# Performance work log

Measured on AMD Instinct MI355X. Metric: run time of the kernel, lower is better.

Reference implementation:

```python
import jax, jax.numpy as jnp
import numpy as np

B, L, C = 4, 2048, 1024
H = 16
D = C // H  # head_dim = 64


def _rope(t, cos, sin):
    # t: [B, H, L, D]; cos/sin: [L, D//2] broadcast to [1, 1, L, D//2]
    te = t[..., ::2]
    to = t[..., 1::2]
    c = cos[None, None]
    s = sin[None, None]
    re = te * c - to * s
    ro = te * s + to * c
    # interleave even/odd back: [..., D//2, 2] -> [..., D]
    return jnp.stack([re, ro], axis=-1).reshape(t.shape)


def setup_inputs() -> dict:
    key = jax.random.key(0)
    ks = jax.random.split(key, 5)
    x = jax.random.normal(ks[0], (B, L, C), dtype=jnp.float32)
    # rotary phases: theta_i = 10000^(-2i/D), angles = pos * theta
    inv_freq = 1.0 / (10000.0 ** (np.arange(0, D, 2, dtype=np.float32) / D))
    ang = np.arange(L, dtype=np.float32)[:, None] * inv_freq[None, :]  # [L, D//2]
    cos = jnp.asarray(np.cos(ang))
    sin = jnp.asarray(np.sin(ang))
    w_qkv = jax.random.normal(ks[1], (3 * C, C), dtype=jnp.float32) * (C ** -0.5)
    w_proj = jax.random.normal(ks[2], (C, C), dtype=jnp.float32) * (C ** -0.5)
    b_proj = jnp.zeros((C,), dtype=jnp.float32)
    return {"x": x, "cos": cos, "sin": sin, "w_qkv": w_qkv, "w_proj": w_proj, "b_proj": b_proj}


def reference(x, cos, sin, w_qkv, w_proj, b_proj):
    Bx, Lx, Cx = x.shape
    # QKV projection (torch Linear: y = x @ W.T), then split heads
    qkv = jnp.einsum("blc,fc->blf", x, w_qkv)  # [B, L, 3C]
    qkv = qkv.reshape(Bx, Lx, 3, H, D).transpose(2, 0, 3, 1, 4)  # [3, B, H, L, D]
    q, k, v = qkv[0], qkv[1], qkv[2]
    q = _rope(q, cos, sin)
    k = _rope(k, cos, sin)
    # scaled dot-product attention, non-causal
    scale = D ** -0.5
    scores = jnp.einsum("bhqd,bhkd->bhqk", q, k) * scale
    attn = jax.nn.softmax(scores, axis=-1)
    o = jnp.einsum("bhqk,bhkd->bhqd", attn, v)  # [B, H, L, D]
    o = o.transpose(0, 2, 1, 3).reshape(Bx, Lx, Cx)
    return jnp.einsum("blc,fc->blf", o, w_proj) + b_proj
```

## Files before the change

### kernel.cpp

```cpp
#include <hip/hip_runtime.h>
#include <hip/hip_bf16.h>
#include <cstdint>


typedef unsigned short u16;
typedef __attribute__((ext_vector_type(8))) short bf16x8;
typedef __attribute__((ext_vector_type(4))) float f32x4;
typedef __attribute__((ext_vector_type(2))) unsigned int u32x2;

#define GLD16(g, l)                                                            \
  __builtin_amdgcn_global_load_lds(                                            \
      (const __attribute__((address_space(1))) void*)(g),                      \
      (__attribute__((address_space(3))) void*)(l), 16, 0, 0)

static __device__ __forceinline__ u16 f32_bf16(float f) {
  union { float f; unsigned u; } v; v.f = f;
  unsigned r = v.u + 0x7FFFu + ((v.u >> 16) & 1u);
  return (u16)(r >> 16);
}
static __device__ __forceinline__ float bf16_f32(u16 h) {
  union { unsigned u; float f; } v; v.u = ((unsigned)h) << 16;
  return v.f;
}
static __device__ __forceinline__ unsigned pack_rne(float a, float b) {
  union { float f; unsigned u; } x, y; x.f = a; y.f = b;
  unsigned ua = x.u + 0x7FFFu + ((x.u >> 16) & 1u);
  unsigned ub = y.u + 0x7FFFu + ((y.u >> 16) & 1u);
  return (ua >> 16) | (ub & 0xFFFF0000u);
}
static __device__ __forceinline__ unsigned pack_bf16_hw(float a, float b) {
  float2 t; t.x = a; t.y = b;
  __hip_bfloat162 h = __float22bfloat162_rn(t);
  union { __hip_bfloat162 h; unsigned u; } c; c.h = h;
  return c.u;
}

__global__ __launch_bounds__(256) void convert_all(
    const void* __restrict__ x, const void* __restrict__ wq,
    const void* __restrict__ wp, const void* __restrict__ cs,
    const void* __restrict__ sn, const void* __restrict__ bs,
    u16* __restrict__ xb, u16* __restrict__ wqb, u16* __restrict__ wpb,
    u16* __restrict__ cb, u16* __restrict__ sb, u16* __restrict__ bb) {
  const unsigned f32mode = (((const unsigned*)cs)[0] == 0x3F800000u);
  int blk = blockIdx.x;
  if (blk >= 12288 && blk < 12416) {
    const void* src = (blk < 12352) ? cs : sn;
    u16* dst = (blk < 12352) ? cb : sb;
    int i = (blk - ((blk < 12352) ? 12288 : 12352)) * 256 + threadIdx.x;
    u16 e[4];
    if (f32mode) {
      float4 v = ((const float4*)src)[i];
      const float* vf = (const float*)&v;
#pragma unroll
      for (int c = 0; c < 4; c++) e[c] = f32_bf16(vf[c]);
    } else {
      uint2 v = ((const uint2*)src)[i];
      e[0] = (u16)(v.x & 0xFFFFu); e[1] = (u16)(v.x >> 16);
      e[2] = (u16)(v.y & 0xFFFFu); e[3] = (u16)(v.y >> 16);
    }
#pragma unroll
    for (int c = 0; c < 4; c++) {
      int E = i * 4 + c;
      dst[(E & 31) * 2048 + (E >> 5)] = e[c];
    }
    return;
  }
  const void* src; u16* dst; int i0, n4;
  bool is_wq = false;
  if (blk < 8192)       { src = x;  dst = xb;  i0 = blk;         n4 = 2097152; }
  else if (blk < 11264) { src = wq; dst = wqb; i0 = blk - 8192;  n4 = 786432; is_wq = true; }
  else if (blk < 12288) { src = wp; dst = wpb; i0 = blk - 11264; n4 = 262144; }
  else                  { src = bs; dst = bb;  i0 = blk - 12416; n4 = 256; }
  int i = i0 * 256 + threadIdx.x;
  if (i >= n4) return;
  int si = i;
  if (is_wq) {
    int f = i >> 8, c4 = i & 255;
    if (f < 2048) {
      int loc = f & 63;
      int srcf = (f & ~63) | ((loc < 32) ? (2 * loc) : (2 * (loc - 32) + 1));
      si = srcf * 256 + c4;
    }
  }
  if (f32mode) {
    float4 v = ((const float4*)src)[si];
    uint2 o;
    o.x = pack_rne(v.x, v.y);
    o.y = pack_rne(v.z, v.w);
    ((uint2*)dst)[i] = o;
  } else {
    ((uint2*)dst)[i] = ((const uint2*)src)[si];
  }
}

static __device__ __forceinline__ void gemm_mainloop(
    const u16* __restrict__ A, const u16* __restrict__ Bm, int K,
    int m0, int n0, u16* As, u16* Bs, f32x4 acc[4][4]) {
  const int tid  = threadIdx.x;
  const int lane = tid & 63;
  const int wave = tid >> 6;
  const int n16  = lane & 15;
  const int quad = lane >> 4;
  const int wm = (wave >> 1) * 64;
  const int wn = (wave & 1) * 64;
  const u16* ag = A  + (size_t)(m0 + wave * 16 + (lane >> 2)) * K + (lane & 3) * 8;
  const u16* bg = Bm + (size_t)(n0 + wave * 16 + (lane >> 2)) * K + (lane & 3) * 8;
  u16* al = As + wave * (16 * 32);
  u16* bl = Bs + wave * (16 * 32);
  GLD16(ag, al);
  GLD16(ag + (size_t)64 * K, al + 64 * 32);
  GLD16(bg, bl);
  GLD16(bg + (size_t)64 * K, bl + 64 * 32);
  for (int kt = 0; kt < K; kt += 32) {
    const int buf = (kt >> 5) & 1;
    __syncthreads();
    if (kt + 32 < K) {
      const int nb = buf ^ 1;
      GLD16(ag + kt + 32, al + nb * 4096);
      GLD16(ag + (size_t)64 * K + kt + 32, al + nb * 4096 + 64 * 32);
      GLD16(bg + kt + 32, bl + nb * 4096);
      GLD16(bg + (size_t)64 * K + kt + 32, bl + nb * 4096 + 64 * 32);
    }
    const u16* as = As + buf * 4096;
    const u16* bs = Bs + buf * 4096;
    bf16x8 af[4], bf[4];
#pragma unroll
    for (int i = 0; i < 4; i++)
      af[i] = *(const bf16x8*)(as + (wm + i * 16 + n16) * 32 + quad * 8);
#pragma unroll
    for (int j = 0; j < 4; j++)
      bf[j] = *(const bf16x8*)(bs + (wn + j * 16 + n16) * 32 + quad * 8);
#pragma unroll
    for (int i = 0; i < 4; i++)
#pragma unroll
      for (int j = 0; j < 4; j++)
        acc[i][j] = __builtin_amdgcn_mfma_f32_16x16x32_bf16(af[i], bf[j], acc[i][j], 0, 0, 0);
  }
}

__global__ __launch_bounds__(256) void gemm_qkv(
    const u16* __restrict__ x, const u16* __restrict__ w,
    u16* __restrict__ q_ws, u16* __restrict__ k_ws, u16* __restrict__ vt_ws,
    const u16* __restrict__ cosT, const u16* __restrict__ sinT) {
  __shared__ u16 As[2 * 128 * 32];
  __shared__ u16 Bs[2 * 128 * 32];
  f32x4 acc[4][4];
#pragma unroll
  for (int i = 0; i < 4; i++)
#pragma unroll
    for (int j = 0; j < 4; j++) acc[i][j] = (f32x4){0.f, 0.f, 0.f, 0.f};
  const int m0 = blockIdx.y * 128;
  const int n0 = blockIdx.x * 128;
  gemm_mainloop(x, w, 1024, m0, n0, As, Bs, acc);
  const int lane = threadIdx.x & 63, wave = threadIdx.x >> 6;
  const int n16 = lane & 15, quad = lane >> 4;
  const int wm = (wave >> 1) * 64, wn = (wave & 1) * 64;
  const int fw = n0 + wn;
  const int which = fw >> 10;
  const int h = (fw & 1023) >> 6;
  if (which == 2) {
#pragma unroll
    for (int i = 0; i < 4; i++)
#pragma unroll
      for (int j = 0; j < 4; j++) {
        int d = j * 16 + n16;
        int l0 = m0 + wm + i * 16 + quad * 4;
        int b = l0 >> 11, l = l0 & 2047;
        uint2 o;
        o.x = pack_bf16_hw(acc[i][j][0], acc[i][j][1]);
        o.y = pack_bf16_hw(acc[i][j][2], acc[i][j][3]);
        size_t idx = (((size_t)b * 16 + h) * 64 + d) * 2048 + l;
        *(uint2*)(vt_ws + idx) = o;
      }
  } else {
    u16* dst = (which == 0) ? q_ws : k_ws;
    const float sc = (which == 0) ? 0.18033688011112042f : 1.0f;
#pragma unroll
    for (int i = 0; i < 4; i++) {
      int l0 = m0 + wm + i * 16 + quad * 4;
      int b = l0 >> 11, l = l0 & 2047;
#pragma unroll
      for (int jj = 0; jj < 2; jj++) {
        int m = jj * 16 + n16;
        uint2 cu = *(const uint2*)(cosT + m * 2048 + l);
        uint2 su = *(const uint2*)(sinT + m * 2048 + l);
        float cf[4] = {bf16_f32((u16)(cu.x & 0xFFFFu)) * sc, bf16_f32((u16)(cu.x >> 16)) * sc,
                       bf16_f32((u16)(cu.y & 0xFFFFu)) * sc, bf16_f32((u16)(cu.y >> 16)) * sc};
        float sf[4] = {bf16_f32((u16)(su.x & 0xFFFFu)) * sc, bf16_f32((u16)(su.x >> 16)) * sc,
                       bf16_f32((u16)(su.y & 0xFFFFu)) * sc, bf16_f32((u16)(su.y >> 16)) * sc};
        size_t base = (((size_t)b * 16 + h) * 2048 + l) * 64 + 2 * m;
#pragma unroll
        for (int r = 0; r < 4; r++) {
          float te = acc[i][jj][r];
          float to = acc[i][jj + 2][r];
          float re = te * cf[r] - to * sf[r];
          float ro = te * sf[r] + to * cf[r];
          *(unsigned*)(dst + base + (size_t)r * 64) = pack_bf16_hw(re, ro);
        }
      }
    }
  }
}

__global__ __launch_bounds__(256, 4) void flash_attn(
    const u16* __restrict__ q_ws, const u16* __restrict__ k_ws,
    const u16* __restrict__ vt_ws, u16* __restrict__ o_ws) {
  __shared__ u16 Ks[2][64 * 64];
  __shared__ u16 Vs[2][64 * 64];
  const int bh = blockIdx.x & 63;
  const int q0 = (blockIdx.x >> 6) * 128;
  const int b = bh >> 4, h = bh & 15;
  const int tid = threadIdx.x, lane = tid & 63, wave = tid >> 6;
  const int n16 = lane & 15, quad = lane >> 4;
  const int x7 = n16 & 7;
  const int pn16 = (n16 & 3) | ((n16 & 4) << 1) | ((n16 & 8) >> 1);
  const int px7 = pn16 & 7;
  const size_t hoff = (size_t)bh * (2048 * 64);

  bf16x8 qf[2][2];
#pragma unroll
  for (int qb = 0; qb < 2; qb++) {
    const u16* qrow = q_ws + hoff + (size_t)(q0 + wave * 32 + qb * 16 + n16) * 64;
    qf[qb][0] = *(const bf16x8*)(qrow + quad * 8);
    qf[qb][1] = *(const bf16x8*)(qrow + 32 + quad * 8);
  }

  f32x4 oacc[2][4];
  f32x4 lq[2];
#pragma unroll
  for (int qb = 0; qb < 2; qb++) {
    lq[qb] = (f32x4){0.f, 0.f, 0.f, 0.f};
#pragma unroll
    for (int s = 0; s < 4; s++) oacc[qb][s] = (f32x4){0.f, 0.f, 0.f, 0.f};
  }

  const int srow = wave * 8 + (lane >> 3);
  const int sw = (lane & 7) ^ ((lane >> 3) & 7);
  const u16* kg = k_ws + hoff + (size_t)srow * 64 + sw * 8;
  const u16* vg = vt_ws + hoff + (size_t)srow * 2048 + sw * 8;
  const int loff = wave * 8 * 64;

  GLD16(kg, &Ks[0][loff]);
  GLD16(kg + 32 * 64, &Ks[0][loff + 32 * 64]);
  GLD16(vg, &Vs[0][loff]);
  GLD16(vg + (size_t)32 * 2048, &Vs[0][loff + 32 * 64]);

  for (int kt = 0; kt < 2048; kt += 64) {
    const int buf = (kt >> 6) & 1;
    __syncthreads();
    if (kt + 64 < 2048) {
      const u16* kgn = kg + (size_t)(kt + 64) * 64;
      const u16* vgn = vg + (kt + 64);
      GLD16(kgn, &Ks[buf ^ 1][loff]);
      GLD16(kgn + 32 * 64, &Ks[buf ^ 1][loff + 32 * 64]);
      GLD16(vgn, &Vs[buf ^ 1][loff]);
      GLD16(vgn + (size_t)32 * 2048, &Vs[buf ^ 1][loff + 32 * 64]);
    }
    const u16* ks = Ks[buf];
    const u16* vs = Vs[buf];

    unsigned pxk[2][4], pyk[2][4];
#pragma unroll
    for (int sub = 0; sub < 4; sub++) {
      const u16* krow = ks + (sub * 16 + pn16) * 64;
      bf16x8 kf0 = *(const bf16x8*)(krow + (quad ^ px7) * 8);
      bf16x8 kf1 = *(const bf16x8*)(krow + ((quad + 4) ^ px7) * 8);
#pragma unroll
      for (int qb = 0; qb < 2; qb++) {
        f32x4 z = (f32x4){0.f, 0.f, 0.f, 0.f};
        z = __builtin_amdgcn_mfma_f32_16x16x32_bf16(kf0, qf[qb][0], z, 0, 0, 0);
        z = __builtin_amdgcn_mfma_f32_16x16x32_bf16(kf1, qf[qb][1], z, 0, 0, 0);
        f32x4 p;
#pragma unroll
        for (int r = 0; r < 4; r++) p[r] = __builtin_amdgcn_exp2f(z[r]);
        lq[qb] += p;
        pxk[qb][sub] = pack_bf16_hw(p[0], p[1]);
        pyk[qb][sub] = pack_bf16_hw(p[2], p[3]);
      }
    }

    bf16x8 pf[2][2];
#pragma unroll
    for (int qb = 0; qb < 2; qb++) {
      u32x2 r0 = __builtin_amdgcn_permlane32_swap(pxk[qb][0], pxk[qb][1], false, false);
      u32x2 r1 = __builtin_amdgcn_permlane32_swap(pyk[qb][0], pyk[qb][1], false, false);
      u32x2 r2 = __builtin_amdgcn_permlane32_swap(pxk[qb][2], pxk[qb][3], false, false);
      u32x2 r3 = __builtin_amdgcn_permlane32_swap(pyk[qb][2], pyk[qb][3], false, false);
      union { unsigned u[4]; bf16x8 v; } t0, t1;
      t0.u[0] = r0.x; t0.u[1] = r1.x; t0.u[2] = r0.y; t0.u[3] = r1.y;
      t1.u[0] = r2.x; t1.u[1] = r3.x; t1.u[2] = r2.y; t1.u[3] = r3.y;
      pf[qb][0] = t0.v;
      pf[qb][1] = t1.v;
    }

#pragma unroll
    for (int sd = 0; sd < 4; sd++) {
      const u16* vrow = vs + (sd * 16 + n16) * 64;
      bf16x8 vf0 = *(const bf16x8*)(vrow + (quad ^ x7) * 8);
      bf16x8 vf1 = *(const bf16x8*)(vrow + ((quad + 4) ^ x7) * 8);
#pragma unroll
      for (int qb = 0; qb < 2; qb++) {
        oacc[qb][sd] = __builtin_amdgcn_mfma_f32_16x16x32_bf16(pf[qb][0], vf0, oacc[qb][sd], 0, 0, 0);
        oacc[qb][sd] = __builtin_amdgcn_mfma_f32_16x16x32_bf16(pf[qb][1], vf1, oacc[qb][sd], 0, 0, 0);
      }
    }
  }

#pragma unroll
  for (int qb = 0; qb < 2; qb++) {
    float l = lq[qb][0] + lq[qb][1] + lq[qb][2] + lq[qb][3];
    l += __shfl_xor(l, 16, 64);
    l += __shfl_xor(l, 32, 64);
    float linv = 1.0f / l;
#pragma unroll
    for (int r = 0; r < 4; r++) {
      float lr = __shfl(linv, quad * 4 + r, 64);
      int row = q0 + wave * 32 + qb * 16 + quad * 4 + r;
      size_t base = ((size_t)b * 2048 + row) * 1024 + h * 64;
#pragma unroll
      for (int sd = 0; sd < 4; sd++)
        o_ws[base + sd * 16 + n16] = f32_bf16(oacc[qb][sd][r] * lr);
    }
  }
}

__global__ __launch_bounds__(256) void gemm_proj(
    const u16* __restrict__ o, const u16* __restrict__ w,
    const u16* __restrict__ bias, float* __restrict__ out) {
  __shared__ u16 As[2 * 128 * 32];
  __shared__ u16 Bs[2 * 128 * 32];
  f32x4 acc[4][4];
#pragma unroll
  for (int i = 0; i < 4; i++)
#pragma unroll
    for (int j = 0; j < 4; j++) acc[i][j] = (f32x4){0.f, 0.f, 0.f, 0.f};
  const int m0 = blockIdx.y * 128;
  const int n0 = blockIdx.x * 128;
  gemm_mainloop(o, w, 1024, m0, n0, As, Bs, acc);
  const int lane = threadIdx.x & 63, wave = threadIdx.x >> 6;
  const int n16 = lane & 15, quad = lane >> 4;
  const int wm = (wave >> 1) * 64, wn = (wave & 1) * 64;
#pragma unroll
  for (int i = 0; i < 4; i++)
#pragma unroll
    for (int j = 0; j < 4; j++) {
      int f = n0 + wn + j * 16 + n16;
      float bf = bf16_f32(bias[f]);
#pragma unroll
      for (int r = 0; r < 4; r++) {
        int m = m0 + wm + i * 16 + quad * 4 + r;
        out[(size_t)m * 1024 + f] = acc[i][j][r] + bf;
      }
    }
}

extern "C" void kernel_launch(void* const* d_in, const int* in_sizes, int n_in,
                              void* d_out, int out_size, void* d_ws, size_t ws_size,
                              hipStream_t stream) {
  float* out = (float*)d_out;

  u16* ws = (u16*)d_ws;
  u16* xb     = ws;
  u16* wqkvb  = ws + 8388608;
  u16* wprojb = ws + 11534336;
  u16* cosb   = ws + 12582912;
  u16* sinb   = ws + 12648448;
  u16* biasb  = ws + 12713984;
  u16* qb     = ws + 12715008;
  u16* kb     = ws + 21103616;
  u16* vtb    = ws + 29492224;
  u16* ob     = xb;

  convert_all<<<12417, 256, 0, stream>>>(
      d_in[0], d_in[3], d_in[4], d_in[1], d_in[2], d_in[5],
      xb, wqkvb, wprojb, cosb, sinb, biasb);

  gemm_qkv<<<dim3(24, 64), 256, 0, stream>>>(xb, wqkvb, qb, kb, vtb, cosb, sinb);
  flash_attn<<<1024, 256, 0, stream>>>(qb, kb, vtb, ob);
  gemm_proj<<<dim3(8, 64), 256, 0, stream>>>(ob, wprojb, biasb, out);
}
```

Measured before the change: 291.9 us.

## Load K/V tiles directly into registers, dropping LDS staging and barriers

```diff
diff --git a/kernel.cpp b/kernel.cpp
--- a/kernel.cpp
+++ b/kernel.cpp
@@ -202,19 +202,66 @@
   }
 }
 
-__global__ __launch_bounds__(256, 4) void flash_attn(
+#define FTILE(KC, KN, KT)                                                      \
+  {                                                                            \
+    _Pragma("unroll")                                                          \
+    for (int sd = 0; sd < 4; sd++) {                                           \
+      vc[sd][0] = *(const bf16x8*)(vpt + (size_t)sd * 32768 + (KT));           \
+      vc[sd][1] = *(const bf16x8*)(vpt + (size_t)sd * 32768 + (KT) + 32);      \
+    }                                                                          \
+    _Pragma("unroll")                                                          \
+    for (int s = 0; s < 4; s++) {                                              \
+      KN[s][0] = *(const bf16x8*)(kpt + (size_t)((KT) + 64 + s * 16) * 64);    \
+      KN[s][1] = *(const bf16x8*)(kpt + (size_t)((KT) + 64 + s * 16) * 64 + 32); \
+    }                                                                          \
+    unsigned pxk[2][4], pyk[2][4];                                             \
+    _Pragma("unroll")                                                          \
+    for (int sub = 0; sub < 4; sub++) {                                        \
+      _Pragma("unroll")                                                        \
+      for (int qb = 0; qb < 2; qb++) {                                         \
+        f32x4 z = (f32x4){0.f, 0.f, 0.f, 0.f};                                 \
+        z = __builtin_amdgcn_mfma_f32_16x16x32_bf16(KC[sub][0], qf[qb][0], z, 0, 0, 0); \
+        z = __builtin_amdgcn_mfma_f32_16x16x32_bf16(KC[sub][1], qf[qb][1], z, 0, 0, 0); \
+        f32x4 p;                                                               \
+        _Pragma("unroll")                                                      \
+        for (int r = 0; r < 4; r++) p[r] = __builtin_amdgcn_exp2f(z[r]);       \
+        lq[qb] += p;                                                           \
+        pxk[qb][sub] = pack_bf16_hw(p[0], p[1]);                               \
+        pyk[qb][sub] = pack_bf16_hw(p[2], p[3]);                               \
+      }                                                                        \
+    }                                                                          \
+    bf16x8 pf[2][2];                                                           \
+    _Pragma("unroll")                                                          \
+    for (int qb = 0; qb < 2; qb++) {                                           \
+      u32x2 r0 = __builtin_amdgcn_permlane32_swap(pxk[qb][0], pxk[qb][1], false, false); \
+      u32x2 r1 = __builtin_amdgcn_permlane32_swap(pyk[qb][0], pyk[qb][1], false, false); \
+      u32x2 r2 = __builtin_amdgcn_permlane32_swap(pxk[qb][2], pxk[qb][3], false, false); \
+      u32x2 r3 = __builtin_amdgcn_permlane32_swap(pyk[qb][2], pyk[qb][3], false, false); \
+      union { unsigned u[4]; bf16x8 v; } t0, t1;                               \
+      t0.u[0] = r0.x; t0.u[1] = r1.x; t0.u[2] = r0.y; t0.u[3] = r1.y;          \
+      t1.u[0] = r2.x; t1.u[1] = r3.x; t1.u[2] = r2.y; t1.u[3] = r3.y;          \
+      pf[qb][0] = t0.v;                                                        \
+      pf[qb][1] = t1.v;                                                        \
+    }                                                                          \
+    _Pragma("unroll")                                                          \
+    for (int sd = 0; sd < 4; sd++) {                                           \
+      _Pragma("unroll")                                                        \
+      for (int qb = 0; qb < 2; qb++) {                                         \
+        oacc[qb][sd] = __builtin_amdgcn_mfma_f32_16x16x32_bf16(pf[qb][0], vc[sd][0], oacc[qb][sd], 0, 0, 0); \
+        oacc[qb][sd] = __builtin_amdgcn_mfma_f32_16x16x32_bf16(pf[qb][1], vc[sd][1], oacc[qb][sd], 0, 0, 0); \
+      }                                                                        \
+    }                                                                          \
+  }
+
+__global__ __launch_bounds__(256, 2) void flash_attn(
     const u16* __restrict__ q_ws, const u16* __restrict__ k_ws,
     const u16* __restrict__ vt_ws, u16* __restrict__ o_ws) {
-  __shared__ u16 Ks[2][64 * 64];
-  __shared__ u16 Vs[2][64 * 64];
   const int bh = blockIdx.x & 63;
   const int q0 = (blockIdx.x >> 6) * 128;
   const int b = bh >> 4, h = bh & 15;
   const int tid = threadIdx.x, lane = tid & 63, wave = tid >> 6;
   const int n16 = lane & 15, quad = lane >> 4;
-  const int x7 = n16 & 7;
   const int pn16 = (n16 & 3) | ((n16 & 4) << 1) | ((n16 & 8) >> 1);
-  const int px7 = pn16 & 7;
   const size_t hoff = (size_t)bh * (2048 * 64);
 
   bf16x8 qf[2][2];
@@ -234,76 +281,20 @@
     for (int s = 0; s < 4; s++) oacc[qb][s] = (f32x4){0.f, 0.f, 0.f, 0.f};
   }
 
-  const int srow = wave * 8 + (lane >> 3);
-  const int sw = (lane & 7) ^ ((lane >> 3) & 7);
-  const u16* kg = k_ws + hoff + (size_t)srow * 64 + sw * 8;
-  const u16* vg = vt_ws + hoff + (size_t)srow * 2048 + sw * 8;
-  const int loff = wave * 8 * 64;
-
-  GLD16(kg, &Ks[0][loff]);
-  GLD16(kg + 32 * 64, &Ks[0][loff + 32 * 64]);
-  GLD16(vg, &Vs[0][loff]);
-  GLD16(vg + (size_t)32 * 2048, &Vs[0][loff + 32 * 64]);
-
-  for (int kt = 0; kt < 2048; kt += 64) {
-    const int buf = (kt >> 6) & 1;
-    __syncthreads();
-    if (kt + 64 < 2048) {
-      const u16* kgn = kg + (size_t)(kt + 64) * 64;
-      const u16* vgn = vg + (kt + 64);
-      GLD16(kgn, &Ks[buf ^ 1][loff]);
-      GLD16(kgn + 32 * 64, &Ks[buf ^ 1][loff + 32 * 64]);
-      GLD16(vgn, &Vs[buf ^ 1][loff]);
-      GLD16(vgn + (size_t)32 * 2048, &Vs[buf ^ 1][loff + 32 * 64]);
-    }
-    const u16* ks = Ks[buf];
-    const u16* vs = Vs[buf];
-
-    unsigned pxk[2][4], pyk[2][4];
-#pragma unroll
-    for (int sub = 0; sub < 4; sub++) {
-      const u16* krow = ks + (sub * 16 + pn16) * 64;
-      bf16x8 kf0 = *(const bf16x8*)(krow + (quad ^ px7) * 8);
-      bf16x8 kf1 = *(const bf16x8*)(krow + ((quad + 4) ^ px7) * 8);
-#pragma unroll
-      for (int qb = 0; qb < 2; qb++) {
-        f32x4 z = (f32x4){0.f, 0.f, 0.f, 0.f};
-        z = __builtin_amdgcn_mfma_f32_16x16x32_bf16(kf0, qf[qb][0], z, 0, 0, 0);
-        z = __builtin_amdgcn_mfma_f32_16x16x32_bf16(kf1, qf[qb][1], z, 0, 0, 0);
-        f32x4 p;
-#pragma unroll
-        for (int r = 0; r < 4; r++) p[r] = __builtin_amdgcn_exp2f(z[r]);
-        lq[qb] += p;
-        pxk[qb][sub] = pack_bf16_hw(p[0], p[1]);
-        pyk[qb][sub] = pack_bf16_hw(p[2], p[3]);
-      }
-    }
-
-    bf16x8 pf[2][2];
-#pragma unroll
-    for (int qb = 0; qb < 2; qb++) {
-      u32x2 r0 = __builtin_amdgcn_permlane32_swap(pxk[qb][0], pxk[qb][1], false, false);
-      u32x2 r1 = __builtin_amdgcn_permlane32_swap(pyk[qb][0], pyk[qb][1], false, false);
-      u32x2 r2 = __builtin_amdgcn_permlane32_swap(pxk[qb][2], pxk[qb][3], false, false);
-      u32x2 r3 = __builtin_amdgcn_permlane32_swap(pyk[qb][2], pyk[qb][3], false, false);
-      union { unsigned u[4]; bf16x8 v; } t0, t1;
-      t0.u[0] = r0.x; t0.u[1] = r1.x; t0.u[2] = r0.y; t0.u[3] = r1.y;
-      t1.u[0] = r2.x; t1.u[1] = r3.x; t1.u[2] = r2.y; t1.u[3] = r3.y;
-      pf[qb][0] = t0.v;
-      pf[qb][1] = t1.v;
-    }
-
-#pragma unroll
-    for (int sd = 0; sd < 4; sd++) {
-      const u16* vrow = vs + (sd * 16 + n16) * 64;
-      bf16x8 vf0 = *(const bf16x8*)(vrow + (quad ^ x7) * 8);
-      bf16x8 vf1 = *(const bf16x8*)(vrow + ((quad + 4) ^ x7) * 8);
-#pragma unroll
-      for (int qb = 0; qb < 2; qb++) {
-        oacc[qb][sd] = __builtin_amdgcn_mfma_f32_16x16x32_bf16(pf[qb][0], vf0, oacc[qb][sd], 0, 0, 0);
-        oacc[qb][sd] = __builtin_amdgcn_mfma_f32_16x16x32_bf16(pf[qb][1], vf1, oacc[qb][sd], 0, 0, 0);
-      }
-    }
+  const u16* kpt = k_ws + hoff + (size_t)pn16 * 64 + quad * 8;
+  const u16* vpt = vt_ws + hoff + (size_t)n16 * 2048 + quad * 8;
+
+  bf16x8 kA[4][2], kB[4][2], vc[4][2];
+#pragma unroll
+  for (int s = 0; s < 4; s++) {
+    kA[s][0] = *(const bf16x8*)(kpt + (size_t)(s * 16) * 64);
+    kA[s][1] = *(const bf16x8*)(kpt + (size_t)(s * 16) * 64 + 32);
+  }
+
+#pragma unroll 1
+  for (int kt = 0; kt < 2048; kt += 128) {
+    FTILE(kA, kB, kt);
+    FTILE(kB, kA, kt + 64);
   }
 
 #pragma unroll
```

After: 494.0 us. 69.2% more time.
